# Performance work log

Measured on AMD Instinct MI355X. Metric: run time of the kernel, lower is better.

## Reference

```python
import jax, jax.numpy as jnp
import numpy as np

L1, L2, N, C = 4096, 4096, 8, 3


def setup_inputs() -> dict:
    key = jax.random.key(0)
    k1, k2 = jax.random.split(key)
    coords1 = jax.random.uniform(k1, (L1, N, C), dtype=jnp.float32)
    coords2 = jax.random.uniform(k2, (L2, N, C), dtype=jnp.float32)
    return {"coords1": coords1, "coords2": coords2}


def reference(coords1, coords2):
    # coords1: [L1, N, C], coords2: [L2, N, C]
    l1, n, c = coords1.shape
    l2 = coords2.shape[0]
    # Batch-first layout, matching flatten_batch semantics (per-batch NN only)
    q = jnp.swapaxes(coords2, 0, 1)  # [N, L2, C] query points
    r = jnp.swapaxes(coords1, 0, 1)  # [N, L1, C] reference points
    # Squared euclidean distances per batch: [N, L2, L1]
    d2 = (
        jnp.sum(q * q, axis=-1)[:, :, None]
        + jnp.sum(r * r, axis=-1)[:, None, :]
        - 2.0 * jnp.einsum("nlc,nmc->nlm", q, r)
    )
    # tc.nearest returns global flat index; original does fmod(L1) to get the
    # per-batch index — argmin within each batch gives that directly.
    nearest = jnp.argmin(d2, axis=-1)  # [N, L2]
    clusters = nearest.T  # [L2, N]
    # torch.meshgrid(arange(L2), arange(N)) with 'ij' indexing; indices[-1] is
    # the batch index broadcast to [L2, N].
    batch_idx = jnp.broadcast_to(jnp.arange(n, dtype=jnp.int64 if False else jnp.int32), (l2, n))
    return (clusters.reshape(-1), batch_idx.reshape(-1))
```

## Files before the change

### kernel.cpp

```cpp
#include <hip/hip_runtime.h>
#include <float.h>


constexpr int kL1 = 4096, kL2 = 4096, kN = 8;
constexpr int kCS = 520;
constexpr size_t kOffPts = 8ull * kCS * 4;
constexpr size_t kWsBytes = kOffPts + 8ull * kL1 * 16;

__device__ __forceinline__ float rr_exact(float x, float y, float z) {
  return __fadd_rn(__fadd_rn(__fmul_rn(x, x), __fmul_rn(y, y)), __fmul_rn(z, z));
}

__global__ __launch_bounds__(1024)
void bin_kernel(const float* __restrict__ c1, int* __restrict__ cellStart,
                float4* __restrict__ pts) {
#pragma clang fp contract(off)
  __shared__ int cnt[512];
  const int tid = threadIdx.x;
  const int n = blockIdx.x;
  if (tid < 512) cnt[tid] = 0;
  __syncthreads();

  float xs[4], ys[4], zs[4];
  int cl[4];
#pragma unroll
  for (int k = 0; k < 4; ++k) {
    const int j = k * 1024 + tid;
    const float* p = c1 + (j * kN + n) * 3;
    const float x = p[0], y = p[1], z = p[2];
    xs[k] = x; ys[k] = y; zs[k] = z;
    const int cx = min(7, max(0, (int)(x * 8.0f)));
    const int cy = min(7, max(0, (int)(y * 8.0f)));
    const int cz = min(7, max(0, (int)(z * 8.0f)));
    cl[k] = (cz * 8 + cy) * 8 + cx;
    atomicAdd(&cnt[cl[k]], 1);
  }
  __syncthreads();

  if (tid < 64) {
    int loc[8], part = 0;
#pragma unroll
    for (int i = 0; i < 8; ++i) { loc[i] = cnt[tid * 8 + i]; part += loc[i]; }
    int inc = part;
#pragma unroll
    for (int off = 1; off < 64; off <<= 1) {
      const int v = __shfl_up(inc, off);
      if (tid >= off) inc += v;
    }
    int base = inc - part;
#pragma unroll
    for (int i = 0; i < 8; ++i) {
      const int c = tid * 8 + i;
      cellStart[n * kCS + c] = base;
      cnt[c] = base;
      base += loc[i];
    }
    if (tid == 0) cellStart[n * kCS + 512] = kL1;
  }
  __syncthreads();

#pragma unroll
  for (int k = 0; k < 4; ++k) {
    const int j = k * 1024 + tid;
    const int pos = atomicAdd(&cnt[cl[k]], 1);
    pts[n * kL1 + pos] =
        make_float4(xs[k], ys[k], zs[k], __int_as_float(j));
  }
}

__global__ __launch_bounds__(256, 8)
void grid_nn_kernel(const int* __restrict__ cellStart, const float4* __restrict__ pts,
                    const float* __restrict__ c2, int* __restrict__ out) {
#pragma clang fp contract(off)
  const int n = blockIdx.y;
  const int wave = threadIdx.x >> 6;
  const int lane = threadIdx.x & 63;
  const int qj = blockIdx.x * 4 + wave;

  const float* p = c2 + (qj * kN + n) * 3;
  const float qx = p[0], qy = p[1], qz = p[2];
  const float qq = rr_exact(qx, qy, qz);
  const int cx = min(7, max(0, (int)(qx * 8.0f)));
  const int cy = min(7, max(0, (int)(qy * 8.0f)));
  const int cz = min(7, max(0, (int)(qz * 8.0f)));
  const int xlo = max(0, cx - 1), xhi = min(7, cx + 1);

  const int* __restrict__ cs = cellStart + n * kCS;
  const float4* __restrict__ P = pts + n * kL1;

  float bd = FLT_MAX;
  int bi = 0x7FFFFFFF;

#pragma unroll
  for (int dz = -1; dz <= 1; ++dz) {
#pragma unroll
    for (int dy = -1; dy <= 1; ++dy) {
      const int z = cz + dz, y = cy + dy;
      if (z < 0 || z > 7 || y < 0 || y > 7) continue;
      const int row = (z * 8 + y) * 8;
      const int s = cs[row + xlo];
      const int e = cs[row + xhi + 1];
      for (int pp = s + lane; pp < e; pp += 64) {
        const float4 rp = P[pp];
        const int id = __float_as_int(rp.w);
        const float rr = rr_exact(rp.x, rp.y, rp.z);
        const float dot = __fadd_rn(
            __fadd_rn(__fmul_rn(qx, rp.x), __fmul_rn(qy, rp.y)),
            __fmul_rn(qz, rp.z));
        const float d2 = __fmaf_rn(-2.0f, dot, __fadd_rn(qq, rr));
        if (d2 < bd || (d2 == bd && id < bi)) { bd = d2; bi = id; }
      }
    }
  }

#pragma unroll
  for (int m = 1; m <= 32; m <<= 1) {
    const float od = __shfl_xor(bd, m);
    const int oi = __shfl_xor(bi, m);
    if (od < bd || (od == bd && oi < bi)) { bd = od; bi = oi; }
  }

  if (!(0.015625f > __fadd_rn(bd, 4e-6f))) {
    for (int pp = lane; pp < kL1; pp += 64) {
      const float4 rp = P[pp];
      const int id = __float_as_int(rp.w);
      const float rr = rr_exact(rp.x, rp.y, rp.z);
      const float dot = __fadd_rn(
          __fadd_rn(__fmul_rn(qx, rp.x), __fmul_rn(qy, rp.y)),
          __fmul_rn(qz, rp.z));
      const float d2 = __fmaf_rn(-2.0f, dot, __fadd_rn(qq, rr));
      if (d2 < bd || (d2 == bd && id < bi)) { bd = d2; bi = id; }
    }
#pragma unroll
    for (int m = 1; m <= 32; m <<= 1) {
      const float od = __shfl_xor(bd, m);
      const int oi = __shfl_xor(bi, m);
      if (od < bd || (od == bd && oi < bi)) { bd = od; bi = oi; }
    }
  }

  if (lane == 0) {
    out[qj * kN + n] = bi;
    out[kL2 * kN + qj * kN + n] = n;
  }
}

constexpr int kQPerBlock = 16;
constexpr int kQ = 4;
constexpr int kChunk = 1024;

__global__ __launch_bounds__(256, 4)
void nearest_kernel_lds(const float* __restrict__ c1, const float* __restrict__ c2,
                        int* __restrict__ out) {
#pragma clang fp contract(off)
  __shared__ float sRx[kChunk], sRy[kChunk], sRz[kChunk], sRr[kChunk];
  const int tid = threadIdx.x;
  const int n = blockIdx.y;
  const int wave = tid >> 6;
  const int lane = tid & 63;
  const int q0 = blockIdx.x * kQPerBlock + wave * kQ;

  float qxs[kQ], qys[kQ], qzs[kQ], qqs[kQ];
#pragma unroll
  for (int i = 0; i < kQ; ++i) {
    const float* p = c2 + ((q0 + i) * kN + n) * 3;
    qxs[i] = p[0]; qys[i] = p[1]; qzs[i] = p[2];
    qqs[i] = rr_exact(qxs[i], qys[i], qzs[i]);
  }
  float bd[kQ]; int bt[kQ];
#pragma unroll
  for (int i = 0; i < kQ; ++i) { bd[i] = FLT_MAX; bt[i] = 0; }

  for (int chunk = 0; chunk < kL1 / kChunk; ++chunk) {
    __syncthreads();
    {
      const int jb = chunk * kChunk + tid * 4;
      float x[4], y[4], z[4], w4[4];
#pragma unroll
      for (int k = 0; k < 4; ++k) {
        const float* p = c1 + ((jb + k) * kN + n) * 3;
        x[k] = p[0]; y[k] = p[1]; z[k] = p[2];
        w4[k] = rr_exact(x[k], y[k], z[k]);
      }
      *reinterpret_cast<float4*>(&sRx[tid * 4]) = make_float4(x[0], x[1], x[2], x[3]);
      *reinterpret_cast<float4*>(&sRy[tid * 4]) = make_float4(y[0], y[1], y[2], y[3]);
      *reinterpret_cast<float4*>(&sRz[tid * 4]) = make_float4(z[0], z[1], z[2], z[3]);
      *reinterpret_cast<float4*>(&sRr[tid * 4]) = make_float4(w4[0], w4[1], w4[2], w4[3]);
    }
    __syncthreads();
#pragma unroll
    for (int t = 0; t < kChunk / 256; ++t) {
      const int tg = chunk * (kChunk / 256) + t;
      const int base = t * 256 + lane * 4;
      const float4 x4 = *reinterpret_cast<const float4*>(&sRx[base]);
      const float4 y4 = *reinterpret_cast<const float4*>(&sRy[base]);
      const float4 z4 = *reinterpret_cast<const float4*>(&sRz[base]);
      const float4 r4 = *reinterpret_cast<const float4*>(&sRr[base]);
      const float xs[4] = {x4.x, x4.y, x4.z, x4.w};
      const float ys[4] = {y4.x, y4.y, y4.z, y4.w};
      const float zs[4] = {z4.x, z4.y, z4.z, z4.w};
      const float rs[4] = {r4.x, r4.y, r4.z, r4.w};
#pragma unroll
      for (int i = 0; i < kQ; ++i) {
        float d[4];
#pragma unroll
        for (int k = 0; k < 4; ++k) {
          const float dot = __fadd_rn(
              __fadd_rn(__fmul_rn(qxs[i], xs[k]), __fmul_rn(qys[i], ys[k])),
              __fmul_rn(qzs[i], zs[k]));
          d[k] = __fmaf_rn(-2.0f, dot, __fadd_rn(qqs[i], rs[k]));
        }
        const float old = bd[i];
        float m = fminf(fminf(d[0], d[1]), old);
        m = fminf(fminf(d[2], d[3]), m);
        bd[i] = m;
        if (m < old) bt[i] = tg;
      }
    }
  }
  int sel[kQ];
#pragma unroll
  for (int i = 0; i < kQ; ++i) sel[i] = bt[i] * 64 + lane;
#pragma unroll
  for (int m = 1; m <= 32; m <<= 1) {
#pragma unroll
    for (int i = 0; i < kQ; ++i) {
      const float od = __shfl_xor(bd[i], m);
      const int os = __shfl_xor(sel[i], m);
      if (od < bd[i] || (od == bd[i] && os < sel[i])) { bd[i] = od; sel[i] = os; }
    }
  }
#pragma unroll
  for (int i = 0; i < kQ; ++i) {
    if (lane == i) {
      const int j0 = sel[i] * 4;
      float best = FLT_MAX; int kk = 0;
#pragma unroll
      for (int k = 0; k < 4; ++k) {
        const float* p = c1 + ((j0 + k) * kN + n) * 3;
        const float r0 = p[0], r1 = p[1], r2 = p[2];
        const float rr = rr_exact(r0, r1, r2);
        const float dot = __fadd_rn(
            __fadd_rn(__fmul_rn(qxs[i], r0), __fmul_rn(qys[i], r1)),
            __fmul_rn(qzs[i], r2));
        const float dc = __fmaf_rn(-2.0f, dot, __fadd_rn(qqs[i], rr));
        if (dc < best) { best = dc; kk = k; }
      }
      out[(q0 + i) * kN + n] = j0 + kk;
      out[kL2 * kN + (q0 + i) * kN + n] = n;
    }
  }
}

extern "C" void kernel_launch(void* const* d_in, const int* in_sizes, int n_in,
                              void* d_out, int out_size, void* d_ws, size_t ws_size,
                              hipStream_t stream) {
  const float* c1 = (const float*)d_in[0];
  const float* c2 = (const float*)d_in[1];
  int* out = (int*)d_out;
  if (d_ws != nullptr && ws_size >= kWsBytes) {
    int* cellStart = (int*)d_ws;
    float4* pts = (float4*)((char*)d_ws + kOffPts);
    bin_kernel<<<dim3(kN), dim3(1024), 0, stream>>>(c1, cellStart, pts);
    grid_nn_kernel<<<dim3(kL2 / 4, kN), dim3(256), 0, stream>>>(
        cellStart, pts, c2, out);
  } else {
    dim3 grid(kL2 / kQPerBlock, kN);
    nearest_kernel_lds<<<grid, dim3(256), 0, stream>>>(c1, c2, out);
  }
}
```

Before: 88.02 us.

## Flatten 9 neighbor-cell ranges into one unrolled loop over all candidates

Each query wave now precomputes the start offset and length of all nine neighbor cell-row ranges, prefix-sums them, and walks the combined candidate list in chunks of 256 with four independent loads per lane. This is meant to remove lane underutilization from short per-row loops and to increase memory-level parallelism by issuing several loads before the compute. In exchange, each candidate pays a 9-way select to map its flat index to an address. The launch bound's occupancy hint also drops from 8 to 6 to leave room for the extra registers.

Result: faster. 82.18 us (-6.6%).

```diff
diff --git a/kernel.cpp b/kernel.cpp
--- a/kernel.cpp
+++ b/kernel.cpp
@@ -1,5 +1,6 @@
 #include <hip/hip_runtime.h>
 #include <float.h>
+#include <limits.h>
 
 
 constexpr int kL1 = 4096, kL2 = 4096, kN = 8;
@@ -63,12 +64,11 @@
   for (int k = 0; k < 4; ++k) {
     const int j = k * 1024 + tid;
     const int pos = atomicAdd(&cnt[cl[k]], 1);
-    pts[n * kL1 + pos] =
-        make_float4(xs[k], ys[k], zs[k], __int_as_float(j));
-  }
-}
-
-__global__ __launch_bounds__(256, 8)
+    pts[n * kL1 + pos] = make_float4(xs[k], ys[k], zs[k], __int_as_float(j));
+  }
+}
+
+__global__ __launch_bounds__(256, 6)
 void grid_nn_kernel(const int* __restrict__ cellStart, const float4* __restrict__ pts,
                     const float* __restrict__ c2, int* __restrict__ out) {
 #pragma clang fp contract(off)
@@ -88,28 +88,52 @@
   const int* __restrict__ cs = cellStart + n * kCS;
   const float4* __restrict__ P = pts + n * kL1;
 
+  int S[9], Lk[9], pre[10];
+#pragma unroll
+  for (int k = 0; k < 9; ++k) {
+    const int dz = k / 3 - 1, dy = k % 3 - 1;
+    const int z = cz + dz, y = cy + dy;
+    const bool valid = ((unsigned)z <= 7u) && ((unsigned)y <= 7u);
+    const int zc = min(7, max(0, z)), yc = min(7, max(0, y));
+    const int row = (zc * 8 + yc) * 8;
+    const int s = cs[row + xlo];
+    const int e = cs[row + xhi + 1];
+    S[k] = s;
+    Lk[k] = valid ? (e - s) : 0;
+  }
+  pre[0] = 0;
+#pragma unroll
+  for (int k = 0; k < 9; ++k) pre[k + 1] = pre[k] + Lk[k];
+  const int T = pre[9];
+
   float bd = FLT_MAX;
-  int bi = 0x7FFFFFFF;
-
-#pragma unroll
-  for (int dz = -1; dz <= 1; ++dz) {
-#pragma unroll
-    for (int dy = -1; dy <= 1; ++dy) {
-      const int z = cz + dz, y = cy + dy;
-      if (z < 0 || z > 7 || y < 0 || y > 7) continue;
-      const int row = (z * 8 + y) * 8;
-      const int s = cs[row + xlo];
-      const int e = cs[row + xhi + 1];
-      for (int pp = s + lane; pp < e; pp += 64) {
-        const float4 rp = P[pp];
-        const int id = __float_as_int(rp.w);
-        const float rr = rr_exact(rp.x, rp.y, rp.z);
-        const float dot = __fadd_rn(
-            __fadd_rn(__fmul_rn(qx, rp.x), __fmul_rn(qy, rp.y)),
-            __fmul_rn(qz, rp.z));
-        const float d2 = __fmaf_rn(-2.0f, dot, __fadd_rn(qq, rr));
-        if (d2 < bd || (d2 == bd && id < bi)) { bd = d2; bi = id; }
-      }
+  int bi = INT_MAX;
+
+  for (int base = 0; base < T; base += 256) {
+    int g[4], a[4];
+#pragma unroll
+    for (int u = 0; u < 4; ++u) {
+      g[u] = base + lane + u * 64;
+      int ad = 0;
+#pragma unroll
+      for (int k = 0; k < 9; ++k) {
+        const bool in = (g[u] >= pre[k]) && (g[u] < pre[k + 1]);
+        ad = in ? (S[k] + (g[u] - pre[k])) : ad;
+      }
+      a[u] = ad;
+    }
+    float4 rp[4];
+#pragma unroll
+    for (int u = 0; u < 4; ++u) rp[u] = P[a[u]];
+#pragma unroll
+    for (int u = 0; u < 4; ++u) {
+      const int id = __float_as_int(rp[u].w);
+      const float rr = rr_exact(rp[u].x, rp[u].y, rp[u].z);
+      const float dot = __fadd_rn(
+          __fadd_rn(__fmul_rn(qx, rp[u].x), __fmul_rn(qy, rp[u].y)),
+          __fmul_rn(qz, rp[u].z));
+      const float d2 = __fmaf_rn(-2.0f, dot, __fadd_rn(qq, rr));
+      if (g[u] < T && (d2 < bd || (d2 == bd && id < bi))) { bd = d2; bi = id; }
     }
   }
 
```

## Bin queries by cell too and use four lanes per query in grid NN

Applied to the files above, without the earlier changes.

The single-block-per-batch binning kernel is split into three wide kernels: cell computation, histogram and scan, and an atomic scatter. The same binning is now applied to query points as well as reference points. The NN kernel then walks queries in cell-sorted order with 4 lanes per query instead of a 64-lane wave, so nearby queries in a wave share reference cells and far fewer lanes sit idle on small cell ranges. This adds two extra kernel launches and atomic global scatters, and the fallback brute-force path now runs on only 4 lanes.

Measured after the change: 88.07 us. About the same (+0.1%).

```diff
diff --git a/kernel.cpp b/kernel.cpp
--- a/kernel.cpp
+++ b/kernel.cpp
@@ -1,46 +1,68 @@
 #include <hip/hip_runtime.h>
 #include <float.h>
+#include <limits.h>
 
 
 constexpr int kL1 = 4096, kL2 = 4096, kN = 8;
 constexpr int kCS = 520;
-constexpr size_t kOffPts = 8ull * kCS * 4;
-constexpr size_t kWsBytes = kOffPts + 8ull * kL1 * 16;
+constexpr size_t kOffCurR = 8ull * kCS * 4;
+constexpr size_t kOffCsQ  = kOffCurR + 8ull * 512 * 4;
+constexpr size_t kOffCurQ = kOffCsQ + 8ull * kCS * 4;
+constexpr size_t kOffCellR = kOffCurQ + 8ull * 512 * 4;
+constexpr size_t kOffCellQ = kOffCellR + 32768ull * 2;
+constexpr size_t kOffPtsR = kOffCellQ + 32768ull * 2;
+constexpr size_t kOffPtsQ = kOffPtsR + 8ull * 4096 * 16;
+constexpr size_t kWsBytes = kOffPtsQ + 8ull * 4096 * 16;
 
 __device__ __forceinline__ float rr_exact(float x, float y, float z) {
   return __fadd_rn(__fadd_rn(__fmul_rn(x, x), __fmul_rn(y, y)), __fmul_rn(z, z));
 }
 
+__device__ __forceinline__ int cell_of(float x, float y, float z) {
+  const int cx = min(7, max(0, (int)(x * 8.0f)));
+  const int cy = min(7, max(0, (int)(y * 8.0f)));
+  const int cz = min(7, max(0, (int)(z * 8.0f)));
+  return (cz * 8 + cy) * 8 + cx;
+}
+
+__global__ __launch_bounds__(256)
+void cellof_kernel(const float* __restrict__ c1, const float* __restrict__ c2,
+                   unsigned short* __restrict__ cellR,
+                   unsigned short* __restrict__ cellQ) {
+  const int t = blockIdx.x * 256 + threadIdx.x;
+  const int u = t & 32767;
+  const float* p = (t < 32768 ? c1 : c2) + 3 * u;
+  const int c = cell_of(p[0], p[1], p[2]);
+  if (t < 32768) cellR[u] = (unsigned short)c;
+  else cellQ[u] = (unsigned short)c;
+}
+
 __global__ __launch_bounds__(1024)
-void bin_kernel(const float* __restrict__ c1, int* __restrict__ cellStart,
-                float4* __restrict__ pts) {
-#pragma clang fp contract(off)
-  __shared__ int cnt[512];
+void histscan_kernel(const unsigned short* __restrict__ cellR,
+                     const unsigned short* __restrict__ cellQ,
+                     int* __restrict__ csR, int* __restrict__ curR,
+                     int* __restrict__ csQ, int* __restrict__ curQ) {
+  __shared__ int hist[512];
   const int tid = threadIdx.x;
-  const int n = blockIdx.x;
-  if (tid < 512) cnt[tid] = 0;
+  const int n = blockIdx.x & 7;
+  const bool isQ = blockIdx.x >= 8;
+  const unsigned short* cof = isQ ? cellQ : cellR;
+  int* cs = isQ ? csQ : csR;
+  int* cur = isQ ? curQ : curR;
+  if (tid < 512) hist[tid] = 0;
   __syncthreads();
 
-  float xs[4], ys[4], zs[4];
-  int cl[4];
 #pragma unroll
   for (int k = 0; k < 4; ++k) {
     const int j = k * 1024 + tid;
-    const float* p = c1 + (j * kN + n) * 3;
-    const float x = p[0], y = p[1], z = p[2];
-    xs[k] = x; ys[k] = y; zs[k] = z;
-    const int cx = min(7, max(0, (int)(x * 8.0f)));
-    const int cy = min(7, max(0, (int)(y * 8.0f)));
-    const int cz = min(7, max(0, (int)(z * 8.0f)));
-    cl[k] = (cz * 8 + cy) * 8 + cx;
-    atomicAdd(&cnt[cl[k]], 1);
+    atomicAdd(&hist[cof[j * kN + n]], 1);
   }
   __syncthreads();
 
   if (tid < 64) {
     int loc[8], part = 0;
 #pragma unroll
-    for (int i = 0; i < 8; ++i) { loc[i] = cnt[tid * 8 + i]; part += loc[i]; }
+    for (int i = 0; i < 8; ++i) { loc[i] = hist[tid * 8 + i]; part += loc[i]; }
     int inc = part;
 #pragma unroll
     for (int off = 1; off < 64; off <<= 1) {
@@ -51,78 +73,66 @@
 #pragma unroll
     for (int i = 0; i < 8; ++i) {
       const int c = tid * 8 + i;
-      cellStart[n * kCS + c] = base;
-      cnt[c] = base;
+      cs[n * kCS + c] = base;
+      cur[n * 512 + c] = base;
       base += loc[i];
     }
-    if (tid == 0) cellStart[n * kCS + 512] = kL1;
-  }
-  __syncthreads();
-
-#pragma unroll
-  for (int k = 0; k < 4; ++k) {
-    const int j = k * 1024 + tid;
-    const int pos = atomicAdd(&cnt[cl[k]], 1);
-    pts[n * kL1 + pos] =
-        make_float4(xs[k], ys[k], zs[k], __int_as_float(j));
-  }
-}
-
-__global__ __launch_bounds__(256, 8)
-void grid_nn_kernel(const int* __restrict__ cellStart, const float4* __restrict__ pts,
-                    const float* __restrict__ c2, int* __restrict__ out) {
+    if (tid == 0) cs[n * kCS + 512] = 4096;
+  }
+}
+
+__global__ __launch_bounds__(256)
+void scatter_kernel(const float* __restrict__ c1, const float* __restrict__ c2,
+                    const unsigned short* __restrict__ cellR,
+                    const unsigned short* __restrict__ cellQ,
+                    int* __restrict__ curR, int* __restrict__ curQ,
+                    float4* __restrict__ ptsR, float4* __restrict__ ptsQ) {
+  const int t = blockIdx.x * 256 + threadIdx.x;
+  const int u = t & 32767;
+  const bool isQ = t >= 32768;
+  const float* p = (isQ ? c2 : c1) + 3 * u;
+  const float x = p[0], y = p[1], z = p[2];
+  const int n = u & 7, j = u >> 3;
+  const int cell = (isQ ? cellQ : cellR)[u];
+  int* cur = isQ ? curQ : curR;
+  float4* pts = isQ ? ptsQ : ptsR;
+  const int pos = atomicAdd(&cur[n * 512 + cell], 1);
+  pts[n * 4096 + pos] = make_float4(x, y, z, __int_as_float(j));
+}
+
+__global__ __launch_bounds__(128)
+void cell_nn_kernel(const int* __restrict__ csR, const float4* __restrict__ ptsR,
+                    const float4* __restrict__ ptsQ, int* __restrict__ out) {
 #pragma clang fp contract(off)
   const int n = blockIdx.y;
-  const int wave = threadIdx.x >> 6;
-  const int lane = threadIdx.x & 63;
-  const int qj = blockIdx.x * 4 + wave;
-
-  const float* p = c2 + (qj * kN + n) * 3;
-  const float qx = p[0], qy = p[1], qz = p[2];
+  const int qslot = blockIdx.x * 32 + (threadIdx.x >> 2);
+  const int sub = threadIdx.x & 3;
+
+  const float4 qp = ptsQ[n * 4096 + qslot];
+  const float qx = qp.x, qy = qp.y, qz = qp.z;
   const float qq = rr_exact(qx, qy, qz);
   const int cx = min(7, max(0, (int)(qx * 8.0f)));
   const int cy = min(7, max(0, (int)(qy * 8.0f)));
   const int cz = min(7, max(0, (int)(qz * 8.0f)));
   const int xlo = max(0, cx - 1), xhi = min(7, cx + 1);
 
-  const int* __restrict__ cs = cellStart + n * kCS;
-  const float4* __restrict__ P = pts + n * kL1;
+  const int* __restrict__ cs = csR + n * kCS;
+  const float4* __restrict__ P = ptsR + n * 4096;
 
   float bd = FLT_MAX;
-  int bi = 0x7FFFFFFF;
-
-#pragma unroll
-  for (int dz = -1; dz <= 1; ++dz) {
-#pragma unroll
-    for (int dy = -1; dy <= 1; ++dy) {
-      const int z = cz + dz, y = cy + dy;
-      if (z < 0 || z > 7 || y < 0 || y > 7) continue;
-      const int row = (z * 8 + y) * 8;
-      const int s = cs[row + xlo];
-      const int e = cs[row + xhi + 1];
-      for (int pp = s + lane; pp < e; pp += 64) {
-        const float4 rp = P[pp];
-        const int id = __float_as_int(rp.w);
-        const float rr = rr_exact(rp.x, rp.y, rp.z);
-        const float dot = __fadd_rn(
-            __fadd_rn(__fmul_rn(qx, rp.x), __fmul_rn(qy, rp.y)),
-            __fmul_rn(qz, rp.z));
-        const float d2 = __fmaf_rn(-2.0f, dot, __fadd_rn(qq, rr));
-        if (d2 < bd || (d2 == bd && id < bi)) { bd = d2; bi = id; }
-      }
-    }
-  }
-
-#pragma unroll
-  for (int m = 1; m <= 32; m <<= 1) {
-    const float od = __shfl_xor(bd, m);
-    const int oi = __shfl_xor(bi, m);
-    if (od < bd || (od == bd && oi < bi)) { bd = od; bi = oi; }
-  }
-
-  if (!(0.015625f > __fadd_rn(bd, 4e-6f))) {
-    for (int pp = lane; pp < kL1; pp += 64) {
-      const float4 rp = P[pp];
+  int bi = INT_MAX;
+
+#pragma unroll
+  for (int k = 0; k < 9; ++k) {
+    const int dz = k / 3 - 1, dy = k % 3 - 1;
+    const int z = cz + dz, y = cy + dy;
+    const bool valid = ((unsigned)z <= 7u) && ((unsigned)y <= 7u);
+    const int zc = min(7, max(0, z)), yc = min(7, max(0, y));
+    const int row = (zc * 8 + yc) * 8;
+    const int s = cs[row + xlo];
+    const int e = valid ? cs[row + xhi + 1] : s;
+    for (int p = s + sub; p < e; p += 4) {
+      const float4 rp = P[p];
       const int id = __float_as_int(rp.w);
       const float rr = rr_exact(rp.x, rp.y, rp.z);
       const float dot = __fadd_rn(
@@ -131,15 +141,36 @@
       const float d2 = __fmaf_rn(-2.0f, dot, __fadd_rn(qq, rr));
       if (d2 < bd || (d2 == bd && id < bi)) { bd = d2; bi = id; }
     }
-#pragma unroll
-    for (int m = 1; m <= 32; m <<= 1) {
+  }
+
+#pragma unroll
+  for (int m = 1; m <= 2; m <<= 1) {
+    const float od = __shfl_xor(bd, m);
+    const int oi = __shfl_xor(bi, m);
+    if (od < bd || (od == bd && oi < bi)) { bd = od; bi = oi; }
+  }
+
+  if (!(0.015625f > __fadd_rn(bd, 4e-6f))) {
+    for (int p = sub; p < kL1; p += 4) {
+      const float4 rp = P[p];
+      const int id = __float_as_int(rp.w);
+      const float rr = rr_exact(rp.x, rp.y, rp.z);
+      const float dot = __fadd_rn(
+          __fadd_rn(__fmul_rn(qx, rp.x), __fmul_rn(qy, rp.y)),
+          __fmul_rn(qz, rp.z));
+      const float d2 = __fmaf_rn(-2.0f, dot, __fadd_rn(qq, rr));
+      if (d2 < bd || (d2 == bd && id < bi)) { bd = d2; bi = id; }
+    }
+#pragma unroll
+    for (int m = 1; m <= 2; m <<= 1) {
       const float od = __shfl_xor(bd, m);
       const int oi = __shfl_xor(bi, m);
       if (od < bd || (od == bd && oi < bi)) { bd = od; bi = oi; }
     }
   }
 
-  if (lane == 0) {
+  if (sub == 0) {
+    const int qj = __float_as_int(qp.w);
     out[qj * kN + n] = bi;
     out[kL2 * kN + qj * kN + n] = n;
   }
@@ -259,11 +290,20 @@
   const float* c2 = (const float*)d_in[1];
   int* out = (int*)d_out;
   if (d_ws != nullptr && ws_size >= kWsBytes) {
-    int* cellStart = (int*)d_ws;
-    float4* pts = (float4*)((char*)d_ws + kOffPts);
-    bin_kernel<<<dim3(kN), dim3(1024), 0, stream>>>(c1, cellStart, pts);
-    grid_nn_kernel<<<dim3(kL2 / 4, kN), dim3(256), 0, stream>>>(
-        cellStart, pts, c2, out);
+    int* csR = (int*)d_ws;
+    int* curR = (int*)((char*)d_ws + kOffCurR);
+    int* csQ = (int*)((char*)d_ws + kOffCsQ);
+    int* curQ = (int*)((char*)d_ws + kOffCurQ);
+    unsigned short* cellR = (unsigned short*)((char*)d_ws + kOffCellR);
+    unsigned short* cellQ = (unsigned short*)((char*)d_ws + kOffCellQ);
+    float4* ptsR = (float4*)((char*)d_ws + kOffPtsR);
+    float4* ptsQ = (float4*)((char*)d_ws + kOffPtsQ);
+    cellof_kernel<<<dim3(256), dim3(256), 0, stream>>>(c1, c2, cellR, cellQ);
+    histscan_kernel<<<dim3(16), dim3(1024), 0, stream>>>(cellR, cellQ, csR, curR,
+                                                         csQ, curQ);
+    scatter_kernel<<<dim3(256), dim3(256), 0, stream>>>(c1, c2, cellR, cellQ,
+                                                        curR, curQ, ptsR, ptsQ);
+    cell_nn_kernel<<<dim3(128, 8), dim3(128), 0, stream>>>(csR, ptsR, ptsQ, out);
   } else {
     dim3 grid(kL2 / kQPerBlock, kN);
     nearest_kernel_lds<<<grid, dim3(256), 0, stream>>>(c1, c2, out);
```
